# Kernel optimization log

Measured on AMD Instinct MI355X. Metric: run time of the kernel, lower is better.

## Reference

```python
import jax, jax.numpy as jnp
import numpy as np

B = 524288      # batch
D = 16          # ds_dim
N = 32          # number of dynamical systems
H = 128         # gating hidden width


def setup_inputs() -> dict:
    key = jax.random.key(0)
    ks = jax.random.split(key, 8)
    x_cur = jax.random.normal(ks[0], (B, D), dtype=jnp.float32)
    W1 = jax.random.normal(ks[1], (H, D), dtype=jnp.float32) * 0.1
    b1 = jax.random.normal(ks[2], (H,), dtype=jnp.float32) * 0.1
    W2 = jax.random.normal(ks[3], (N, H), dtype=jnp.float32) * 0.1
    b2 = jax.random.normal(ks[4], (N,), dtype=jnp.float32) * 0.1
    # B matrices are PSD (geotorch.positive_semidefinite), C are skew-symmetric (geotorch.skew)
    Braw = jax.random.normal(ks[5], (N, D, D), dtype=jnp.float32) * 0.3
    B_mats = jnp.einsum('nij,nkj->nik', Braw, Braw)  # PSD: R R^T
    Craw = jax.random.normal(ks[6], (N, D, D), dtype=jnp.float32) * 0.3
    C_mats = 0.5 * (Craw - jnp.swapaxes(Craw, -1, -2))  # skew-symmetric
    x_target = jax.random.normal(ks[7], (1, D), dtype=jnp.float32)
    return {"x_cur": x_cur, "W1": W1, "b1": b1, "W2": W2, "b2": b2,
            "B_mats": B_mats, "C_mats": C_mats, "x_target": x_target}


def reference(x_cur, W1, b1, W2, b2, B_mats, C_mats, x_target):
    # gating weights: softmax(Linear -> ReLU -> Linear)
    h = jax.nn.relu(x_cur @ W1.T + b1)          # [B, H]
    w_all = jax.nn.softmax(h @ W2.T + b2, axis=1)  # [B, N]
    # per-system linear map A_i = B_i + C_i applied to (x* - x)
    A = B_mats + C_mats                          # [N, D, D]
    diff = x_target - x_cur                      # [B, D]
    # torch.mm(A, diff.T).T == diff @ A.T -> proj[b,n,k] = sum_d A[n,k,d] diff[b,d]
    proj = jnp.einsum('nkd,bd->bnk', A, diff)    # [B, N, D]
    out = jnp.einsum('bn,bnk->bk', w_all, proj)  # [B, D]
    return out
```

## Files before the change

### kernel.cpp

```cpp
#include <hip/hip_runtime.h>

#define BATCH 524288

typedef __bf16 bf16x8 __attribute__((ext_vector_type(8)));
typedef __bf16 bf16x2 __attribute__((ext_vector_type(2)));
typedef float f32x4 __attribute__((ext_vector_type(4)));
typedef float f32x8 __attribute__((ext_vector_type(8)));
typedef float f32x2 __attribute__((ext_vector_type(2)));

#define SMEM_BYTES (28704 + 4 * 1088)

__device__ __forceinline__ f32x8 load8(const float* __restrict__ p) {
    float4 a = *(const float4*)p;
    float4 b = *(const float4*)(p + 4);
    f32x8 v = {a.x, a.y, a.z, a.w, b.x, b.y, b.z, b.w};
    return v;
}

__device__ __forceinline__ int pack2bf(float a, float b) {
    f32x2 v = {a, b};
    bf16x2 p = __builtin_convertvector(v, bf16x2);
    return __builtin_bit_cast(int, p);
}

__global__ __launch_bounds__(256, 4) void andp_v6(
    const float* __restrict__ x_cur,
    const float* __restrict__ W1,
    const float* __restrict__ b1,
    const float* __restrict__ W2,
    const float* __restrict__ b2,
    const float* __restrict__ Bm,
    const float* __restrict__ Cm,
    const float* __restrict__ x_t,
    float* __restrict__ out)
{
    extern __shared__ char smem[];
    int* sA2i = (int*)smem;
    int* sW1i = (int*)(smem + 16384);
    int* sW2i = (int*)(smem + 20512);
    const int tid = threadIdx.x;

#pragma unroll
    for (int i = 0; i < 16; ++i) {
        int o2 = tid + i * 256;
        int o  = o2 * 2;
        int kk = o >> 9, k = (o >> 5) & 15, qp = (o >> 3) & 3, j = o & 7;
        int n = 2 * kk + (qp >> 1), d = (qp & 1) * 8 + j;
        int src = n * 256 + k * 16 + d;
        float2 bv = *(const float2*)(Bm + src);
        float2 cv = *(const float2*)(Cm + src);
        sA2i[o2] = pack2bf(bv.x + cv.x, bv.y + cv.y);
    }
#pragma unroll
    for (int i = 0; i < 4; ++i) {
        int p0 = tid + i * 256;
        float2 v = *(const float2*)(W1 + 2 * p0);
        sW1i[p0] = pack2bf(v.x, v.y);
    }
    if (tid < 8) sW1i[1024 + tid] = 0;
#pragma unroll
    for (int i = 0; i < 8; ++i) {
        int o2 = tid + i * 256;
        int chunk = o2 >> 8, r = o2 & 255;
        int ln = r >> 2, j2 = r & 3;
        int q = ln >> 4, cc = ln & 15;
        int t2 = chunk >> 2, kk = chunk & 3;
        int src = (t2 * 16 + cc) * 128 + kk * 32 + q * 8 + j2 * 2;
        float2 v = *(const float2*)(W2 + src);
        sW2i[o2] = pack2bf(v.x, v.y);
    }

    const int wave = tid >> 6, lane = tid & 63;
    const int c = lane & 15, q = lane >> 4;
    const int qh = q >> 1;
    const int hh = (q & 1) * 8;
    const int c4 = c * 4;
    const int sh = qh ? 0 : 16;

    const char* sW1f = smem + 16384;
    const int w1base = (q < 2) ? (c * 32 + q * 16) : 4096;
    const int w1step = (q < 2) ? 512 : 0;
    const char* sW2f = smem + 20512 + lane * 16;
    __bf16* hcw = (__bf16*)(smem + 28704 + wave * 1088);

    float b1v[8];
#pragma unroll
    for (int t = 0; t < 8; ++t) b1v[t] = b1[t * 16 + c];
    float b2v[2][4];
#pragma unroll
    for (int t2 = 0; t2 < 2; ++t2)
#pragma unroll
        for (int r = 0; r < 4; ++r) b2v[t2][r] = b2[t2 * 16 + q * 4 + r];
    const f32x8 xtv = load8(x_t + hh);

    __syncthreads();

    const int blk_row = blockIdx.x * 256 + wave * 64;
    const f32x4 z4 = {0.f, 0.f, 0.f, 0.f};

#pragma unroll 1
    for (int p = 0; p < 2; ++p) {
        const int r0 = blk_row + p * 32;

        bf16x8 af[2];
        f32x8 dif[2];
#pragma unroll
        for (int t01 = 0; t01 < 2; ++t01) {
            f32x8 xv = load8(x_cur + (size_t)(r0 + t01 * 16 + c) * 16 + hh);
            af[t01]  = __builtin_convertvector(xv, bf16x8);
            dif[t01] = xtv - xv;
        }

        int wpk[2][4];

#pragma unroll
        for (int t01 = 0; t01 < 2; ++t01) {
            f32x4 acc2[2];
            acc2[0] = z4; acc2[1] = z4;
#pragma unroll
            for (int th = 0; th < 4; ++th) {
                bf16x8 w1a = *(const bf16x8*)(sW1f + w1base + (2 * th) * w1step);
                bf16x8 w1b = *(const bf16x8*)(sW1f + w1base + (2 * th + 1) * w1step);
                f32x4 a1a = __builtin_amdgcn_mfma_f32_16x16x32_bf16(af[t01], w1a, z4, 0, 0, 0);
                f32x4 a1b = __builtin_amdgcn_mfma_f32_16x16x32_bf16(af[t01], w1b, z4, 0, 0, 0);
#pragma unroll
                for (int r = 0; r < 4; ++r) {
                    float va = fmaxf(a1a[r] + b1v[2 * th], 0.f);
                    float vb = fmaxf(a1b[r] + b1v[2 * th + 1], 0.f);
                    hcw[(q * 4 + r) * 34 + c]      = (__bf16)va;
                    hcw[(q * 4 + r) * 34 + 16 + c] = (__bf16)vb;
                }
                bf16x8 hb = *(const bf16x8*)(hcw + c * 34 + q * 8);
                bf16x8 w20 = *(const bf16x8*)(sW2f + (0 * 4 + th) * 1024);
                bf16x8 w21 = *(const bf16x8*)(sW2f + (1 * 4 + th) * 1024);
                acc2[0] = __builtin_amdgcn_mfma_f32_16x16x32_bf16(w20, hb, acc2[0], 0, 0, 0);
                acc2[1] = __builtin_amdgcn_mfma_f32_16x16x32_bf16(w21, hb, acc2[1], 0, 0, 0);
            }

            float e[8], s = 0.f;
#pragma unroll
            for (int t2 = 0; t2 < 2; ++t2)
#pragma unroll
                for (int r = 0; r < 4; ++r) {
                    e[t2 * 4 + r] = __expf(acc2[t2][r] + b2v[t2][r]);
                    s += e[t2 * 4 + r];
                }
            s += __shfl_xor(s, 16, 64);
            s += __shfl_xor(s, 32, 64);
            float inv = 1.0f / s;
#pragma unroll
            for (int t2 = 0; t2 < 2; ++t2)
#pragma unroll
                for (int rp = 0; rp < 2; ++rp)
                    wpk[t01][t2 * 2 + rp] =
                        pack2bf(e[t2 * 4 + 2 * rp] * inv, e[t2 * 4 + 2 * rp + 1] * inv);
        }

        f32x4 acc3[2];
        acc3[0] = z4; acc3[1] = z4;
#pragma unroll
        for (int kk = 0; kk < 16; ++kk) {
            const int widx = (kk >> 3) * 2 + (kk & 1);
            const int bpi = c4 + ((kk >> 1) & 3) * 64;
            int bp0 = __builtin_amdgcn_ds_bpermute(bpi, wpk[0][widx]);
            int bp1 = __builtin_amdgcn_ds_bpermute(bpi, wpk[1][widx]);
            float w0 = __builtin_bit_cast(float, (unsigned)(bp0 << sh) & 0xffff0000u);
            float w1 = __builtin_bit_cast(float, (unsigned)(bp1 << sh) & 0xffff0000u);
            bf16x8 a2f = *(const bf16x8*)(smem + kk * 1024 + (c * 4 + q) * 16);
            bf16x8 g0 = __builtin_convertvector(dif[0] * w0, bf16x8);
            bf16x8 g1 = __builtin_convertvector(dif[1] * w1, bf16x8);
            acc3[0] = __builtin_amdgcn_mfma_f32_16x16x32_bf16(a2f, g0, acc3[0], 0, 0, 0);
            acc3[1] = __builtin_amdgcn_mfma_f32_16x16x32_bf16(a2f, g1, acc3[1], 0, 0, 0);
        }

#pragma unroll
        for (int t01 = 0; t01 < 2; ++t01) {
            float4 st = make_float4(acc3[t01][0], acc3[t01][1], acc3[t01][2], acc3[t01][3]);
            *(float4*)(out + (size_t)(r0 + t01 * 16 + c) * 16 + q * 4) = st;
        }
    }
}

extern "C" void kernel_launch(void* const* d_in, const int* in_sizes, int n_in,
                              void* d_out, int out_size, void* d_ws, size_t ws_size,
                              hipStream_t stream) {
    const float* x_cur = (const float*)d_in[0];
    const float* W1    = (const float*)d_in[1];
    const float* b1    = (const float*)d_in[2];
    const float* W2    = (const float*)d_in[3];
    const float* b2    = (const float*)d_in[4];
    const float* Bm    = (const float*)d_in[5];
    const float* Cm    = (const float*)d_in[6];
    const float* x_t   = (const float*)d_in[7];
    float* out = (float*)d_out;

    const int blocks = BATCH / 256;
    andp_v6<<<blocks, 256, SMEM_BYTES, stream>>>(
        x_cur, W1, b1, W2, b2, Bm, Cm, x_t, out);
}
```

Measured before the change: 131.1 us.

## Prefetch inputs, interleave row tiles in gating MLP, repack softmax weights

Loads all x_cur rows for both passes up front so global latency overlaps with compute. Interleaves the two 16-row tiles within each hidden-chunk step, using separate LDS scratch buffers, so MFMA chains for the two tiles can overlap. Hidden activations are written as packed bf16 pairs with a padded stride, which requires permuting the W2 staging layout to match. Softmax weights for both tiles are packed into one int, so each k-step selects between two bpermutes rather than shifting per tile. The cost is more LDS per block and more live registers, which may reduce occupancy.

```diff
diff --git a/kernel.cpp b/kernel.cpp
--- a/kernel.cpp
+++ b/kernel.cpp
@@ -8,7 +8,7 @@
 typedef float f32x8 __attribute__((ext_vector_type(8)));
 typedef float f32x2 __attribute__((ext_vector_type(2)));
 
-#define SMEM_BYTES (28704 + 4 * 1088)
+#define SMEM_BYTES (28704 + 4 * 2560)
 
 __device__ __forceinline__ f32x8 load8(const float* __restrict__ p) {
     float4 a = *(const float4*)p;
@@ -23,7 +23,7 @@
     return __builtin_bit_cast(int, p);
 }
 
-__global__ __launch_bounds__(256, 4) void andp_v6(
+__global__ __launch_bounds__(256, 4) void andp_v8(
     const float* __restrict__ x_cur,
     const float* __restrict__ W1,
     const float* __restrict__ b1,
@@ -61,13 +61,12 @@
 #pragma unroll
     for (int i = 0; i < 8; ++i) {
         int o2 = tid + i * 256;
-        int chunk = o2 >> 8, r = o2 & 255;
-        int ln = r >> 2, j2 = r & 3;
-        int q = ln >> 4, cc = ln & 15;
-        int t2 = chunk >> 2, kk = chunk & 3;
-        int src = (t2 * 16 + cc) * 128 + kk * 32 + q * 8 + j2 * 2;
-        float2 v = *(const float2*)(W2 + src);
-        sW2i[o2] = pack2bf(v.x, v.y);
+        int chunk = o2 >> 8, rem = o2 & 255;
+        int ln = rem >> 2, j2 = rem & 3;
+        int qq = ln >> 4, cc = ln & 15;
+        int t2 = chunk >> 2, s = chunk & 3;
+        int src = (t2 * 16 + cc) * 128 + s * 32 + 4 * qq + j2;
+        sW2i[o2] = pack2bf(W2[src], W2[src + 16]);
     }
 
     const int wave = tid >> 6, lane = tid & 63;
@@ -75,13 +74,13 @@
     const int qh = q >> 1;
     const int hh = (q & 1) * 8;
     const int c4 = c * 4;
-    const int sh = qh ? 0 : 16;
 
     const char* sW1f = smem + 16384;
     const int w1base = (q < 2) ? (c * 32 + q * 16) : 4096;
     const int w1step = (q < 2) ? 512 : 0;
     const char* sW2f = smem + 20512 + lane * 16;
-    __bf16* hcw = (__bf16*)(smem + 28704 + wave * 1088);
+    __bf16* hcw0 = (__bf16*)(smem + 28704 + wave * 2560);
+    __bf16* hcw1 = hcw0 + 640;
 
     float b1v[8];
 #pragma unroll
@@ -97,6 +96,13 @@
 
     const int blk_row = blockIdx.x * 256 + wave * 64;
     const f32x4 z4 = {0.f, 0.f, 0.f, 0.f};
+
+    f32x8 xv[2][2];
+#pragma unroll
+    for (int p = 0; p < 2; ++p)
+#pragma unroll
+        for (int t01 = 0; t01 < 2; ++t01)
+            xv[p][t01] = load8(x_cur + (size_t)(blk_row + p * 32 + t01 * 16 + c) * 16 + hh);
 
 #pragma unroll 1
     for (int p = 0; p < 2; ++p) {
@@ -106,66 +112,74 @@
         f32x8 dif[2];
 #pragma unroll
         for (int t01 = 0; t01 < 2; ++t01) {
-            f32x8 xv = load8(x_cur + (size_t)(r0 + t01 * 16 + c) * 16 + hh);
-            af[t01]  = __builtin_convertvector(xv, bf16x8);
-            dif[t01] = xtv - xv;
-        }
-
-        int wpk[2][4];
-
-#pragma unroll
-        for (int t01 = 0; t01 < 2; ++t01) {
-            f32x4 acc2[2];
-            acc2[0] = z4; acc2[1] = z4;
-#pragma unroll
-            for (int th = 0; th < 4; ++th) {
-                bf16x8 w1a = *(const bf16x8*)(sW1f + w1base + (2 * th) * w1step);
-                bf16x8 w1b = *(const bf16x8*)(sW1f + w1base + (2 * th + 1) * w1step);
+            af[t01]  = __builtin_convertvector(xv[p][t01], bf16x8);
+            dif[t01] = xtv - xv[p][t01];
+        }
+
+        f32x4 acc2[2][2];
+        acc2[0][0] = z4; acc2[0][1] = z4; acc2[1][0] = z4; acc2[1][1] = z4;
+#pragma unroll
+        for (int s = 0; s < 4; ++s) {
+#pragma unroll
+            for (int t01 = 0; t01 < 2; ++t01) {
+                __bf16* hcw = t01 ? hcw1 : hcw0;
+                bf16x8 w1a = *(const bf16x8*)(sW1f + w1base + (2 * s) * w1step);
+                bf16x8 w1b = *(const bf16x8*)(sW1f + w1base + (2 * s + 1) * w1step);
                 f32x4 a1a = __builtin_amdgcn_mfma_f32_16x16x32_bf16(af[t01], w1a, z4, 0, 0, 0);
                 f32x4 a1b = __builtin_amdgcn_mfma_f32_16x16x32_bf16(af[t01], w1b, z4, 0, 0, 0);
 #pragma unroll
                 for (int r = 0; r < 4; ++r) {
-                    float va = fmaxf(a1a[r] + b1v[2 * th], 0.f);
-                    float vb = fmaxf(a1b[r] + b1v[2 * th + 1], 0.f);
-                    hcw[(q * 4 + r) * 34 + c]      = (__bf16)va;
-                    hcw[(q * 4 + r) * 34 + 16 + c] = (__bf16)vb;
+                    float va = fmaxf(a1a[r] + b1v[2 * s], 0.f);
+                    float vb = fmaxf(a1b[r] + b1v[2 * s + 1], 0.f);
+                    *(int*)(hcw + (q * 4 + r) * 40 + 2 * c) = pack2bf(va, vb);
                 }
-                bf16x8 hb = *(const bf16x8*)(hcw + c * 34 + q * 8);
-                bf16x8 w20 = *(const bf16x8*)(sW2f + (0 * 4 + th) * 1024);
-                bf16x8 w21 = *(const bf16x8*)(sW2f + (1 * 4 + th) * 1024);
-                acc2[0] = __builtin_amdgcn_mfma_f32_16x16x32_bf16(w20, hb, acc2[0], 0, 0, 0);
-                acc2[1] = __builtin_amdgcn_mfma_f32_16x16x32_bf16(w21, hb, acc2[1], 0, 0, 0);
             }
-
-            float e[8], s = 0.f;
+#pragma unroll
+            for (int t01 = 0; t01 < 2; ++t01) {
+                __bf16* hcw = t01 ? hcw1 : hcw0;
+                bf16x8 hb = *(const bf16x8*)(hcw + c * 40 + q * 8);
+                bf16x8 w20 = *(const bf16x8*)(sW2f + (0 * 4 + s) * 1024);
+                bf16x8 w21 = *(const bf16x8*)(sW2f + (1 * 4 + s) * 1024);
+                acc2[t01][0] = __builtin_amdgcn_mfma_f32_16x16x32_bf16(w20, hb, acc2[t01][0], 0, 0, 0);
+                acc2[t01][1] = __builtin_amdgcn_mfma_f32_16x16x32_bf16(w21, hb, acc2[t01][1], 0, 0, 0);
+            }
+        }
+
+        int wq[8];
+        float w0f[8];
+#pragma unroll
+        for (int t01 = 0; t01 < 2; ++t01) {
+            float e[8], sum = 0.f;
 #pragma unroll
             for (int t2 = 0; t2 < 2; ++t2)
 #pragma unroll
                 for (int r = 0; r < 4; ++r) {
-                    e[t2 * 4 + r] = __expf(acc2[t2][r] + b2v[t2][r]);
-                    s += e[t2 * 4 + r];
+                    e[t2 * 4 + r] = __expf(acc2[t01][t2][r] + b2v[t2][r]);
+                    sum += e[t2 * 4 + r];
                 }
-            s += __shfl_xor(s, 16, 64);
-            s += __shfl_xor(s, 32, 64);
-            float inv = 1.0f / s;
-#pragma unroll
-            for (int t2 = 0; t2 < 2; ++t2)
-#pragma unroll
-                for (int rp = 0; rp < 2; ++rp)
-                    wpk[t01][t2 * 2 + rp] =
-                        pack2bf(e[t2 * 4 + 2 * rp] * inv, e[t2 * 4 + 2 * rp + 1] * inv);
+            sum += __shfl_xor(sum, 16, 64);
+            sum += __shfl_xor(sum, 32, 64);
+            float inv = 1.0f / sum;
+            if (t01 == 0) {
+#pragma unroll
+                for (int i = 0; i < 8; ++i) w0f[i] = e[i] * inv;
+            } else {
+#pragma unroll
+                for (int i = 0; i < 8; ++i) wq[i] = pack2bf(w0f[i], e[i] * inv);
+            }
         }
 
         f32x4 acc3[2];
         acc3[0] = z4; acc3[1] = z4;
 #pragma unroll
         for (int kk = 0; kk < 16; ++kk) {
-            const int widx = (kk >> 3) * 2 + (kk & 1);
+            const int lo = (kk >> 3) * 4 + 2 * (kk & 1);
             const int bpi = c4 + ((kk >> 1) & 3) * 64;
-            int bp0 = __builtin_amdgcn_ds_bpermute(bpi, wpk[0][widx]);
-            int bp1 = __builtin_amdgcn_ds_bpermute(bpi, wpk[1][widx]);
-            float w0 = __builtin_bit_cast(float, (unsigned)(bp0 << sh) & 0xffff0000u);
-            float w1 = __builtin_bit_cast(float, (unsigned)(bp1 << sh) & 0xffff0000u);
+            int bpA = __builtin_amdgcn_ds_bpermute(bpi, wq[lo]);
+            int bpB = __builtin_amdgcn_ds_bpermute(bpi, wq[lo + 1]);
+            int sel = qh ? bpB : bpA;
+            float w0 = __builtin_bit_cast(float, (unsigned)sel << 16);
+            float w1 = __builtin_bit_cast(float, (unsigned)sel & 0xffff0000u);
             bf16x8 a2f = *(const bf16x8*)(smem + kk * 1024 + (c * 4 + q) * 16);
             bf16x8 g0 = __builtin_convertvector(dif[0] * w0, bf16x8);
             bf16x8 g1 = __builtin_convertvector(dif[1] * w1, bf16x8);
@@ -195,6 +209,6 @@
     float* out = (float*)d_out;
 
     const int blocks = BATCH / 256;
-    andp_v6<<<blocks, 256, SMEM_BYTES, stream>>>(
+    andp_v8<<<blocks, 256, SMEM_BYTES, stream>>>(
         x_cur, W1, b1, W2, b2, Bm, Cm, x_t, out);
 }
```

New measurement: 151.3 us. 1.15x slower.
